# Performance work log

Hardware: AMD Instinct MI355X
Metric: run time of the kernel (lower is better)

## Reference

```python
import jax, jax.numpy as jnp
import numpy as np

B, S, HID = 2, 2048, 2048
H = 16           # num_attention_heads
DH = 192         # head_dim
DR = 64          # qk_rope_head_dim
DN = DH - DR     # qk_nope_head_dim
Q_LORA = 512
ROPE_THETA = 10000.0
EPS = 1e-6


def setup_inputs() -> dict:
    key = jax.random.key(0)
    ks = jax.random.split(key, 8)
    scale = 0.02
    x = jax.random.normal(ks[0], (B, S, HID), dtype=jnp.float32)
    position_ids = jnp.broadcast_to(jnp.arange(S, dtype=jnp.int64), (B, S))
    w_qa = jax.random.normal(ks[1], (HID, Q_LORA), dtype=jnp.float32) * scale
    q_norm_w = jnp.ones((Q_LORA,), dtype=jnp.float32)
    w_qb = jax.random.normal(ks[2], (Q_LORA, H * DH), dtype=jnp.float32) * scale
    w_k = jax.random.normal(ks[3], (HID, DH), dtype=jnp.float32) * scale
    w_v = jax.random.normal(ks[4], (HID, DH), dtype=jnp.float32) * scale
    w_o = jax.random.normal(ks[5], (H * DH, HID), dtype=jnp.float32) * scale
    attn_sink = jax.random.normal(ks[6], (H,), dtype=jnp.float32)
    return {"x": x, "w_qa": w_qa, "q_norm_w": q_norm_w, "w_qb": w_qb,
            "w_k": w_k, "w_v": w_v, "w_o": w_o, "attn_sink": attn_sink,
            "position_ids": position_ids}


def _rms_norm(h, w):
    var = jnp.mean(jnp.square(h), axis=-1, keepdims=True)
    return h * jax.lax.rsqrt(var + EPS) * w


def _rotate_half(t):
    t1, t2 = jnp.split(t, 2, axis=-1)
    return jnp.concatenate([-t2, t1], axis=-1)


def _rope_cos_sin(position_ids, dtype):
    inv_freq = 1.0 / (ROPE_THETA ** (jnp.arange(0, DR, 2, dtype=jnp.float32) / DR))
    freqs = position_ids.astype(jnp.float32)[:, :, None] * inv_freq[None, None, :]  # [B,S,DR/2]
    emb = jnp.concatenate([freqs, freqs], axis=-1)  # [B,S,DR]
    return jnp.cos(emb).astype(dtype), jnp.sin(emb).astype(dtype)


def reference(x, w_qa, q_norm_w, w_qb, w_k, w_v, w_o, attn_sink, position_ids):
    b, s, _ = x.shape
    # Low-rank Q path: q_a -> RMSNorm -> q_b, reshape to heads
    q_a = _rms_norm(x @ w_qa, q_norm_w)                      # [B,S,Q_LORA]
    q = (q_a @ w_qb).reshape(b, s, H, DH).transpose(0, 2, 1, 3)  # [B,H,S,DH]
    # MQA single KV head
    k = (x @ w_k)[:, None]                                    # [B,1,S,DH]
    v = (x @ w_v)[:, None]                                    # [B,1,S,DH]
    # Decoupled RoPE on trailing DR dims of q and k
    cos, sin = _rope_cos_sin(position_ids, x.dtype)           # [B,S,DR]
    cos4, sin4 = cos[:, None], sin[:, None]                   # [B,1,S,DR]
    q_nope, q_rope = q[..., :DN], q[..., DN:]
    k_nope, k_rope = k[..., :DN], k[..., DN:]
    q_rope = q_rope * cos4 + _rotate_half(q_rope) * sin4
    k_rope = k_rope * cos4 + _rotate_half(k_rope) * sin4
    q = jnp.concatenate([q_nope, q_rope], axis=-1)
    k = jnp.concatenate([k_nope, k_rope], axis=-1)
    # Attention with learned sink logit
    scaling = DH ** -0.5
    scores = jnp.einsum("bhsd,bgtd->bhst", q, k) * scaling    # [B,H,S,S]
    neg_inf = jnp.finfo(scores.dtype).min
    causal = jnp.tril(jnp.ones((s, s), dtype=bool))
    scores = jnp.where(causal[None, None], scores, neg_inf)
    sink = jnp.broadcast_to(attn_sink.reshape(1, H, 1, 1), (b, H, s, 1)).astype(scores.dtype)
    scores = jnp.concatenate([scores, sink], axis=-1)         # [B,H,S,S+1]
    probs = jax.nn.softmax(scores, axis=-1)[..., :-1]          # drop sink column
    attn = jnp.einsum("bhst,bgtd->bhsd", probs, v)            # [B,H,S,DH]
    attn = attn.transpose(0, 2, 1, 3).reshape(b, s, H * DH)
    return attn @ w_o
```

## Files before the change

### kernel.cpp

```cpp
#include <hip/hip_runtime.h>
#include <hip/hip_bf16.h>

typedef __bf16 bf16_t;
typedef __bf16 bf16x8 __attribute__((ext_vector_type(8)));
typedef __bf16 bf16x4 __attribute__((ext_vector_type(4)));
typedef float  f32x4  __attribute__((ext_vector_type(4)));
typedef __attribute__((address_space(3))) unsigned int lds_u32_t;
typedef __attribute__((address_space(1))) const unsigned int glb_u32_t;

#define B_    2
#define S_    2048
#define HID_  2048
#define H_    16
#define DH_   192
#define DR_   64
#define DN_   128
#define QL_   512
#define NROWS (B_*S_)
#define QKD   (H_*DH_)

#if __has_builtin(__builtin_amdgcn_exp2f)
#define EXP2(x) __builtin_amdgcn_exp2f(x)
#else
#define EXP2(x) exp2f(x)
#endif

__device__ inline void xcd_remap(int& bx, int& by) {
  const int gx = gridDim.x;
  const int nwg = gx * gridDim.y;
  const int flat = by * gx + bx;
  const int q = nwg >> 3;
  const int nf = (flat & 7) * q + (flat >> 3);
  bx = nf % gx;
  by = nf / gx;
}

__global__ void cast_f32_to_bf16(const float* __restrict__ in, bf16_t* __restrict__ out, int n4) {
  int i = blockIdx.x * blockDim.x + threadIdx.x;
  if (i >= n4) return;
  const float4 v = reinterpret_cast<const float4*>(in)[i];
  bf16x4 r;
  r[0] = (bf16_t)v.x; r[1] = (bf16_t)v.y; r[2] = (bf16_t)v.z; r[3] = (bf16_t)v.w;
  reinterpret_cast<bf16x4*>(out)[i] = r;
}

__global__ __launch_bounds__(256) void transpose_all(
    const float* __restrict__ i0, const float* __restrict__ i1,
    const float* __restrict__ i2, const float* __restrict__ i3,
    const float* __restrict__ i4,
    bf16_t* __restrict__ o0, bf16_t* __restrict__ o1, bf16_t* __restrict__ o2,
    bf16_t* __restrict__ o3, bf16_t* __restrict__ o4) {
  int id = blockIdx.x;
  const float* in; bf16_t* out; int R, C, lid;
  if (id < 1024)      { in = i0; out = o0; R = 2048; C = 512;  lid = id; }
  else if (id < 2560) { in = i1; out = o1; R = 512;  C = 3072; lid = id - 1024; }
  else if (id < 2944) { in = i2; out = o2; R = 2048; C = 192;  lid = id - 2560; }
  else if (id < 3328) { in = i3; out = o3; R = 2048; C = 192;  lid = id - 2944; }
  else                { in = i4; out = o4; R = 3072; C = 2048; lid = id - 3328; }
  const int cw = C >> 5;
  const int c0 = (lid % cw) * 32, r0 = (lid / cw) * 32;
  __shared__ float t[32][33];
  const int tx = threadIdx.x & 31;
  const int ty = threadIdx.x >> 5;
#pragma unroll
  for (int j = 0; j < 4; ++j)
    t[ty + j * 8][tx] = in[(size_t)(r0 + ty + j * 8) * C + c0 + tx];
  __syncthreads();
#pragma unroll
  for (int j = 0; j < 4; ++j)
    out[(size_t)(c0 + ty + j * 8) * R + r0 + tx] = (bf16_t)t[tx][ty + j * 8];
}

#define BM 64
#define BN 64
#define BK 64
#define LDT 72

__global__ __launch_bounds__(256) void gemm_kv_kernel(
    const bf16_t* __restrict__ A, const bf16_t* __restrict__ BT,
    bf16_t* __restrict__ Kout, bf16_t* __restrict__ VTout) {
  __shared__ __align__(16) bf16_t sA[BM][LDT];
  __shared__ __align__(16) bf16_t sB[BN][LDT];
  const int tid = threadIdx.x;
  const int w  = tid >> 6;
  const int l  = tid & 63;
  const int lg = l >> 4, lr = l & 15;
  int bx = blockIdx.x, by = blockIdx.y;
  xcd_remap(bx, by);
  const int m0 = by * BM, n0 = bx * BN;
  const int K = HID_;

  f32x4 acc[4];
#pragma unroll
  for (int c = 0; c < 4; ++c) acc[c] = f32x4{0.f, 0.f, 0.f, 0.f};

  for (int k0 = 0; k0 < K; k0 += BK) {
#pragma unroll
    for (int i = 0; i < 2; ++i) {
      int cid = tid + i * 256;
      int row = cid >> 3;
      int cb  = (cid & 7) * 8;
      *reinterpret_cast<uint4*>(&sA[row][cb]) =
          *reinterpret_cast<const uint4*>(&A[(size_t)(m0 + row) * K + k0 + cb]);
      *reinterpret_cast<uint4*>(&sB[row][cb]) =
          *reinterpret_cast<const uint4*>(&BT[(size_t)(n0 + row) * K + k0 + cb]);
    }
    __syncthreads();
#pragma unroll
    for (int ks = 0; ks < 2; ++ks) {
      bf16x8 af = *reinterpret_cast<const bf16x8*>(&sA[w * 16 + lr][ks * 32 + lg * 8]);
#pragma unroll
      for (int c = 0; c < 4; ++c) {
        bf16x8 bfr = *reinterpret_cast<const bf16x8*>(&sB[c * 16 + lr][ks * 32 + lg * 8]);
        acc[c] = __builtin_amdgcn_mfma_f32_16x16x32_bf16(af, bfr, acc[c], 0, 0, 0);
      }
    }
    __syncthreads();
  }
#pragma unroll
  for (int c = 0; c < 4; ++c) {
#pragma unroll
    for (int r = 0; r < 4; ++r) {
      int row = m0 + w * 16 + lg * 4 + r;
      int col = n0 + c * 16 + lr;
      float v = acc[c][r];
      if (col < DH_) Kout[(size_t)row * DH_ + col] = (bf16_t)v;
      else           VTout[(size_t)(col - DH_) * NROWS + row] = (bf16_t)v;
    }
  }
}

template<int OMODE>
__global__ __launch_bounds__(256) void gemm128_kernel(
    const bf16_t* __restrict__ A, const bf16_t* __restrict__ BT,
    void* __restrict__ C, int M, int N, int K, float oscale) {
  __shared__ __align__(16) bf16_t sA[128 * 64];
  __shared__ __align__(16) bf16_t sB[128 * 64];
  const int tid = threadIdx.x;
  const int w  = tid >> 6;
  const int l  = tid & 63;
  const int lg = l >> 4, lr = l & 15;
  const int wm = w >> 1, wn = w & 1;
  int bx = blockIdx.x, by = blockIdx.y;
  xcd_remap(bx, by);
  const int m0 = by * 128, n0 = bx * 128;

  size_t aoff[4], boff[4];
  int ldsoff[4];
#pragma unroll
  for (int i = 0; i < 4; ++i) {
    int cid = i * 256 + tid;
    int row = cid >> 3, ch = cid & 7;
    int sch = ch ^ (row & 7);
    aoff[i] = (size_t)(m0 + row) * K + sch * 8;
    boff[i] = (size_t)(n0 + row) * K + sch * 8;
    ldsoff[i] = (i * 256 + w * 64) * 8;
  }

  f32x4 acc[4][4];
#pragma unroll
  for (int mi = 0; mi < 4; ++mi)
#pragma unroll
    for (int ni = 0; ni < 4; ++ni) acc[mi][ni] = f32x4{0.f, 0.f, 0.f, 0.f};

  for (int k0 = 0; k0 < K; k0 += 64) {
#pragma unroll
    for (int i = 0; i < 4; ++i) {
      __builtin_amdgcn_global_load_lds((glb_u32_t*)(A + aoff[i] + k0),
                                       (lds_u32_t*)(sA + ldsoff[i]), 16, 0, 0);
      __builtin_amdgcn_global_load_lds((glb_u32_t*)(BT + boff[i] + k0),
                                       (lds_u32_t*)(sB + ldsoff[i]), 16, 0, 0);
    }
    asm volatile("s_waitcnt vmcnt(0)" ::: "memory");
    __syncthreads();

#pragma unroll
    for (int ks = 0; ks < 2; ++ks) {
      bf16x8 af[4], bfr[4];
#pragma unroll
      for (int mi = 0; mi < 4; ++mi) {
        int row = wm * 64 + mi * 16 + lr;
        af[mi] = *reinterpret_cast<const bf16x8*>(
            sA + row * 64 + (((ks * 4 + lg) ^ (row & 7)) << 3));
      }
#pragma unroll
      for (int ni = 0; ni < 4; ++ni) {
        int row = wn * 64 + ni * 16 + lr;
        bfr[ni] = *reinterpret_cast<const bf16x8*>(
            sB + row * 64 + (((ks * 4 + lg) ^ (row & 7)) << 3));
      }
#pragma unroll
      for (int mi = 0; mi < 4; ++mi)
#pragma unroll
        for (int ni = 0; ni < 4; ++ni)
          acc[mi][ni] = __builtin_amdgcn_mfma_f32_16x16x32_bf16(af[mi], bfr[ni], acc[mi][ni], 0, 0, 0);
    }
    __syncthreads();
  }

#pragma unroll
  for (int mi = 0; mi < 4; ++mi) {
#pragma unroll
    for (int ni = 0; ni < 4; ++ni) {
#pragma unroll
      for (int r = 0; r < 4; ++r) {
        int row = m0 + wm * 64 + mi * 16 + lg * 4 + r;
        int col = n0 + wn * 64 + ni * 16 + lr;
        float v = acc[mi][ni][r];
        if (OMODE == 0) ((float*)C)[(size_t)row * N + col]  = v;
        else            ((bf16_t*)C)[(size_t)row * N + col] = (bf16_t)(v * oscale);
      }
    }
  }
}

template<int OMODE>
__global__ __launch_bounds__(256) void gemm64x128_kernel(
    const bf16_t* __restrict__ A, const bf16_t* __restrict__ BT,
    void* __restrict__ C, int M, int N, int K, float oscale) {
  __shared__ __align__(16) bf16_t sA[64 * 64];
  __shared__ __align__(16) bf16_t sB[128 * 64];
  const int tid = threadIdx.x;
  const int w  = tid >> 6;
  const int l  = tid & 63;
  const int lg = l >> 4, lr = l & 15;
  const int wm = w >> 1, wn = w & 1;
  int bx = blockIdx.x, by = blockIdx.y;
  xcd_remap(bx, by);
  const int m0 = by * 64, n0 = bx * 128;

  size_t aoff[2], boff[4];
  int ldsa[2], ldsb[4];
#pragma unroll
  for (int i = 0; i < 2; ++i) {
    int cid = i * 256 + tid;
    int row = cid >> 3, ch = cid & 7;
    aoff[i] = (size_t)(m0 + row) * K + (ch ^ (row & 7)) * 8;
    ldsa[i] = (i * 256 + w * 64) * 8;
  }
#pragma unroll
  for (int i = 0; i < 4; ++i) {
    int cid = i * 256 + tid;
    int row = cid >> 3, ch = cid & 7;
    boff[i] = (size_t)(n0 + row) * K + (ch ^ (row & 7)) * 8;
    ldsb[i] = (i * 256 + w * 64) * 8;
  }

  f32x4 acc[2][4];
#pragma unroll
  for (int mi = 0; mi < 2; ++mi)
#pragma unroll
    for (int ni = 0; ni < 4; ++ni) acc[mi][ni] = f32x4{0.f, 0.f, 0.f, 0.f};

  for (int k0 = 0; k0 < K; k0 += 64) {
#pragma unroll
    for (int i = 0; i < 2; ++i)
      __builtin_amdgcn_global_load_lds((glb_u32_t*)(A + aoff[i] + k0),
                                       (lds_u32_t*)(sA + ldsa[i]), 16, 0, 0);
#pragma unroll
    for (int i = 0; i < 4; ++i)
      __builtin_amdgcn_global_load_lds((glb_u32_t*)(BT + boff[i] + k0),
                                       (lds_u32_t*)(sB + ldsb[i]), 16, 0, 0);
    asm volatile("s_waitcnt vmcnt(0)" ::: "memory");
    __syncthreads();

#pragma unroll
    for (int ks = 0; ks < 2; ++ks) {
      bf16x8 af[2], bfr[4];
#pragma unroll
      for (int mi = 0; mi < 2; ++mi) {
        int row = wm * 32 + mi * 16 + lr;
        af[mi] = *reinterpret_cast<const bf16x8*>(
            sA + row * 64 + (((ks * 4 + lg) ^ (row & 7)) << 3));
      }
#pragma unroll
      for (int ni = 0; ni < 4; ++ni) {
        int row = wn * 64 + ni * 16 + lr;
        bfr[ni] = *reinterpret_cast<const bf16x8*>(
            sB + row * 64 + (((ks * 4 + lg) ^ (row & 7)) << 3));
      }
#pragma unroll
      for (int mi = 0; mi < 2; ++mi)
#pragma unroll
        for (int ni = 0; ni < 4; ++ni)
          acc[mi][ni] = __builtin_amdgcn_mfma_f32_16x16x32_bf16(af[mi], bfr[ni], acc[mi][ni], 0, 0, 0);
    }
    __syncthreads();
  }

#pragma unroll
  for (int mi = 0; mi < 2; ++mi) {
#pragma unroll
    for (int ni = 0; ni < 4; ++ni) {
#pragma unroll
      for (int r = 0; r < 4; ++r) {
        int row = m0 + wm * 32 + mi * 16 + lg * 4 + r;
        int col = n0 + wn * 64 + ni * 16 + lr;
        float v = acc[mi][ni][r];
        if (OMODE == 0) ((float*)C)[(size_t)row * N + col]  = v;
        else            ((bf16_t*)C)[(size_t)row * N + col] = (bf16_t)(v * oscale);
      }
    }
  }
}

__global__ __launch_bounds__(64) void rmsnorm_kernel(bf16_t* __restrict__ qa,
                                                     const float* __restrict__ wnorm) {
  int row = blockIdx.x;
  int l = threadIdx.x;
  bf16x8 v = *reinterpret_cast<const bf16x8*>(&qa[(size_t)row * QL_ + l * 8]);
  float f[8];
  float ss = 0.f;
#pragma unroll
  for (int e = 0; e < 8; ++e) { f[e] = (float)v[e]; ss += f[e] * f[e]; }
#pragma unroll
  for (int off = 32; off >= 1; off >>= 1) ss += __shfl_xor(ss, off);
  float rstd = rsqrtf(ss * (1.0f / 512.0f) + 1e-6f);
  bf16x8 o;
#pragma unroll
  for (int e = 0; e < 8; ++e) o[e] = (bf16_t)(f[e] * rstd * wnorm[l * 8 + e]);
  *reinterpret_cast<bf16x8*>(&qa[(size_t)row * QL_ + l * 8]) = o;
}

__global__ void rope_kernel(bf16_t* __restrict__ q, bf16_t* __restrict__ k) {
  int idx = blockIdx.x * blockDim.x + threadIdx.x;
  const int NQ = NROWS * H_ * 32;
  if (idx < NQ) {
    int d   = idx & 31;
    int h   = (idx >> 5) & 15;
    int row = idx >> 9;
    int s = row & (S_ - 1);
    float freq = (float)s * expf(-(float)d * (9.210340371976184f / 32.0f));
    float sn, cs;
    sincosf(freq, &sn, &cs);
    size_t base = (size_t)row * QKD + h * DH_ + DN_ + d;
    float q1 = (float)q[base], q2 = (float)q[base + 32];
    q[base]      = (bf16_t)(q1 * cs - q2 * sn);
    q[base + 32] = (bf16_t)(q2 * cs + q1 * sn);
  } else {
    int i2 = idx - NQ;
    if (i2 >= NROWS * 32) return;
    int d   = i2 & 31;
    int row = i2 >> 5;
    int s = row & (S_ - 1);
    float freq = (float)s * expf(-(float)d * (9.210340371976184f / 32.0f));
    float sn, cs;
    sincosf(freq, &sn, &cs);
    size_t base = (size_t)row * DH_ + DN_ + d;
    float k1 = (float)k[base], k2 = (float)k[base + 32];
    k[base]      = (bf16_t)(k1 * cs - k2 * sn);
    k[base + 32] = (bf16_t)(k2 * cs + k1 * sn);
  }
}

#define KB32  32
#define SPLD  40

__global__ __launch_bounds__(256, 2) void attn_kernel(
    const bf16_t* __restrict__ q, const bf16_t* __restrict__ k,
    const bf16_t* __restrict__ vt, const float* __restrict__ sink,
    bf16_t* __restrict__ attn) {
  __shared__ __align__(16) bf16_t sK[2][KB32 * DH_];
  __shared__ __align__(16) bf16_t sV[DH_ * KB32];
  __shared__ __align__(16) bf16_t sP[4][32][SPLD];
  const int tid = threadIdx.x;
  const int w  = tid >> 6;
  const int l  = tid & 63;
  const int lg = l >> 4, lr = l & 15;
  const int qx = blockIdx.x >> 5;
  const int qt = (qx < 8) ? (15 - qx) : (qx - 8);
  const int bh = blockIdx.x & 31;
  const int b  = bh >> 4, h = bh & 15;
  const int wrow0 = qt * 128 + w * 32;
  const int ktmax_w = 4 * qt + w;
  const int ktmax_b = 4 * qt + 3;

  const bf16_t* kb  = k  + (size_t)(b * S_) * DH_;
  const bf16_t* vtb = vt + (size_t)(b * S_);

  int koff[3], voff[3], ldst[3];
#pragma unroll
  for (int i = 0; i < 3; ++i) {
    int g = i * 256 + tid;
    int krow = g / 24, kch = g - krow * 24;
    koff[i] = krow * DH_ + ((kch ^ (krow & 7)) << 3);
    int vrow = g >> 2, vch = g & 3;
    voff[i] = vrow * NROWS + ((vch ^ (vrow & 3)) << 3);
    ldst[i] = (i * 256 + w * 64) * 8;
  }

  auto stageK = [&](int kt, int bu) {
    const bf16_t* ksrc = kb + (size_t)kt * KB32 * DH_;
#pragma unroll
    for (int i = 0; i < 3; ++i)
      __builtin_amdgcn_global_load_lds((glb_u32_t*)(ksrc + koff[i]),
                                       (lds_u32_t*)(&sK[bu][0] + ldst[i]), 16, 0, 0);
  };
  auto stageV = [&](int kt) {
    const bf16_t* vsrc = vtb + kt * KB32;
#pragma unroll
    for (int i = 0; i < 3; ++i)
      __builtin_amdgcn_global_load_lds((glb_u32_t*)(vsrc + voff[i]),
                                       (lds_u32_t*)(sV + ldst[i]), 16, 0, 0);
  };

  bf16x8 qf[2][6];
#pragma unroll
  for (int rf = 0; rf < 2; ++rf) {
    size_t rowoff = (size_t)(b * S_ + wrow0 + rf * 16 + lr) * QKD + h * DH_;
#pragma unroll
    for (int ks = 0; ks < 6; ++ks)
      qf[rf][ks] = *reinterpret_cast<const bf16x8*>(&q[rowoff + ks * 32 + lg * 8]);
  }

  bf16x8 vones;
#pragma unroll
  for (int e = 0; e < 8; ++e) vones[e] = (bf16_t)((lr == 0) ? 1.0f : 0.0f);

  f32x4 acc[2][13];
#pragma unroll
  for (int rf = 0; rf < 2; ++rf) {
#pragma unroll
    for (int c = 0; c < 12; ++c) acc[rf][c] = f32x4{0.f, 0.f, 0.f, 0.f};
    float init = (lr == 0) ? 1.0f : 0.0f;
    acc[rf][12] = f32x4{init, init, init, init};
  }

  const float L2E = 1.4426950408889634f;
  float m[2][4];
  float sk2 = sink[h] * L2E;
#pragma unroll
  for (int rf = 0; rf < 2; ++rf)
#pragma unroll
    for (int r = 0; r < 4; ++r) m[rf][r] = sk2;

  stageK(0, 0);
  int cur = 0;

  for (int kt = 0; kt <= ktmax_b; ++kt) {
    __syncthreads();

    stageV(kt);
    const bool more = (kt < ktmax_b);
    if (more) stageK(kt + 1, cur ^ 1);

    if (kt <= ktmax_w) {
      if (more) { asm volatile("s_waitcnt vmcnt(6)" ::: "memory"); }
      else      { asm volatile("s_waitcnt vmcnt(3)" ::: "memory"); }

      f32x4 sc[2][2];
#pragma unroll
      for (int rf = 0; rf < 2; ++rf)
#pragma unroll
        for (int c = 0; c < 2; ++c) sc[rf][c] = f32x4{0.f, 0.f, 0.f, 0.f};
#pragma unroll
      for (int c = 0; c < 2; ++c) {
        const int row = c * 16 + lr;
        const int rx  = row & 7;
        const bf16_t* kr = &sK[cur][0] + row * DH_;
#pragma unroll
        for (int ks = 0; ks < 6; ++ks) {
          bf16x8 kf = *reinterpret_cast<const bf16x8*>(kr + (((ks * 4 + lg) ^ rx) << 3));
          sc[0][c] = __builtin_amdgcn_mfma_f32_16x16x32_bf16(qf[0][ks], kf, sc[0][c], 0, 0, 0);
          sc[1][c] = __builtin_amdgcn_mfma_f32_16x16x32_bf16(qf[1][ks], kf, sc[1][c], 0, 0, 0);
        }
      }

      if (kt == ktmax_w) {
#pragma unroll
        for (int rf = 0; rf < 2; ++rf)
#pragma unroll
          for (int c = 0; c < 2; ++c)
#pragma unroll
            for (int r = 0; r < 4; ++r)
              if ((kt * 32 + c * 16 + lr) > (wrow0 + rf * 16 + lg * 4 + r))
                sc[rf][c][r] = -1e30f;
      }

      int ok = 1;
      float lmax[2][4];
#pragma unroll
      for (int rf = 0; rf < 2; ++rf)
#pragma unroll
        for (int r = 0; r < 4; ++r) {
          lmax[rf][r] = fmaxf(sc[rf][0][r], sc[rf][1][r]);
          ok &= (lmax[rf][r] <= m[rf][r] + 8.0f);
        }
      if (!__all(ok)) {
#pragma unroll
        for (int rf = 0; rf < 2; ++rf) {
          float rmax[4], alpha[4];
#pragma unroll
          for (int r = 0; r < 4; ++r) rmax[r] = lmax[rf][r];
#pragma unroll
          for (int off = 1; off < 16; off <<= 1) {
#pragma unroll
            for (int r = 0; r < 4; ++r) rmax[r] = fmaxf(rmax[r], __shfl_xor(rmax[r], off));
          }
#pragma unroll
          for (int r = 0; r < 4; ++r) {
            float mn = fmaxf(m[rf][r], rmax[r]);
            alpha[r] = EXP2(m[rf][r] - mn);
            m[rf][r] = mn;
          }
#pragma unroll
          for (int c = 0; c < 13; ++c)
#pragma unroll
            for (int r = 0; r < 4; ++r) acc[rf][c][r] *= alpha[r];
        }
      }

#pragma unroll
      for (int rf = 0; rf < 2; ++rf)
#pragma unroll
        for (int c = 0; c < 2; ++c)
#pragma unroll
          for (int r = 0; r < 4; ++r)
            sP[w][rf * 16 + lg * 4 + r][c * 16 + lr] = (bf16_t)EXP2(sc[rf][c][r] - m[rf][r]);

      if (more) { asm volatile("s_waitcnt vmcnt(3)" ::: "memory"); }
      else      { asm volatile("s_waitcnt vmcnt(0)" ::: "memory"); }

      bf16x8 pf[2];
      pf[0] = *reinterpret_cast<const bf16x8*>(&sP[w][lr][lg * 8]);
      pf[1] = *reinterpret_cast<const bf16x8*>(&sP[w][16 + lr][lg * 8]);
#pragma unroll
      for (int c2 = 0; c2 < 12; ++c2) {
        const int row = c2 * 16 + lr;
        bf16x8 vf = *reinterpret_cast<const bf16x8*>(
            sV + row * KB32 + ((lg ^ (row & 3)) << 3));
        acc[0][c2] = __builtin_amdgcn_mfma_f32_16x16x32_bf16(pf[0], vf, acc[0][c2], 0, 0, 0);
        acc[1][c2] = __builtin_amdgcn_mfma_f32_16x16x32_bf16(pf[1], vf, acc[1][c2], 0, 0, 0);
      }
      acc[0][12] = __builtin_amdgcn_mfma_f32_16x16x32_bf16(pf[0], vones, acc[0][12], 0, 0, 0);
      acc[1][12] = __builtin_amdgcn_mfma_f32_16x16x32_bf16(pf[1], vones, acc[1][12], 0, 0, 0);
    }
    cur ^= 1;
  }

#pragma unroll
  for (int rf = 0; rf < 2; ++rf) {
    float rl[4];
#pragma unroll
    for (int r = 0; r < 4; ++r) rl[r] = 1.0f / __shfl(acc[rf][12][r], l & 48);
#pragma unroll
    for (int c2 = 0; c2 < 12; ++c2) {
#pragma unroll
      for (int r = 0; r < 4; ++r) {
        int i = wrow0 + rf * 16 + lg * 4 + r;
        size_t off = (size_t)(b * S_ + i) * QKD + h * DH_ + c2 * 16 + lr;
        attn[off] = (bf16_t)(acc[rf][c2][r] * rl[r]);
      }
    }
  }
}

extern "C" void kernel_launch(void* const* d_in, const int* in_sizes, int n_in,
                              void* d_out, int out_size, void* d_ws, size_t ws_size,
                              hipStream_t stream) {
  const float* x        = (const float*)d_in[0];
  const float* w_qa     = (const float*)d_in[1];
  const float* q_norm_w = (const float*)d_in[2];
  const float* w_qb     = (const float*)d_in[3];
  const float* w_k      = (const float*)d_in[4];
  const float* w_v      = (const float*)d_in[5];
  const float* w_o      = (const float*)d_in[6];
  const float* attn_sink= (const float*)d_in[7];
  float* out = (float*)d_out;

  char* ws = (char*)d_ws;
  size_t off = 0;
  auto alloc = [&](size_t bytes) -> void* {
    void* p = ws + off;
    off += (bytes + 255) & ~(size_t)255;
    return p;
  };
  bf16_t* q_b  = (bf16_t*)alloc((size_t)NROWS * QKD * 2);
  bf16_t* k_b  = (bf16_t*)alloc((size_t)NROWS * DH_ * 2);
  bf16_t* vt_b = (bf16_t*)alloc((size_t)DH_ * NROWS * 2);
  bf16_t* wo_t = (bf16_t*)alloc((size_t)HID_ * QKD * 2);
  size_t temp_start = off;
  bf16_t* xb    = (bf16_t*)alloc((size_t)NROWS * HID_ * 2);
  bf16_t* wqa_t = (bf16_t*)alloc((size_t)QL_ * HID_ * 2);
  bf16_t* wqb_t = (bf16_t*)alloc((size_t)QKD * QL_ * 2);
  bf16_t* wkv_t = (bf16_t*)alloc((size_t)(2 * DH_) * HID_ * 2);
  bf16_t* qa_b  = (bf16_t*)alloc((size_t)NROWS * QL_ * 2);
  bf16_t* attn_b = (bf16_t*)(ws + temp_start);

  const float SCALE2 = 0.10411754646447386f;

  int n4x = (int)((size_t)NROWS * HID_ / 4);
  cast_f32_to_bf16<<<dim3((n4x + 255) / 256), dim3(256), 0, stream>>>(x, xb, n4x);
  transpose_all<<<dim3(9472), dim3(256), 0, stream>>>(
      w_qa, w_qb, w_k, w_v, w_o,
      wqa_t, wqb_t, wkv_t, wkv_t + (size_t)DH_ * HID_, wo_t);

  gemm64x128_kernel<1><<<dim3(QL_ / 128, NROWS / 64), 256, 0, stream>>>(xb, wqa_t, qa_b, NROWS, QL_, HID_, 1.0f);
  rmsnorm_kernel<<<dim3(NROWS), dim3(64), 0, stream>>>(qa_b, q_norm_w);
  gemm128_kernel<1><<<dim3(QKD / 128, NROWS / 128), 256, 0, stream>>>(qa_b, wqb_t, q_b, NROWS, QKD, QL_, SCALE2);
  gemm_kv_kernel<<<dim3((2 * DH_) / BN, NROWS / BM), 256, 0, stream>>>(xb, wkv_t, k_b, vt_b);
  {
    int total = NROWS * (H_ + 1) * 32;
    rope_kernel<<<dim3((total + 255) / 256), dim3(256), 0, stream>>>(q_b, k_b);
  }
  attn_kernel<<<dim3(512), dim3(256), 0, stream>>>(q_b, k_b, vt_b, attn_sink, attn_b);
  gemm64x128_kernel<0><<<dim3(HID_ / 128, NROWS / 64), 256, 0, stream>>>(attn_b, wo_t, out, NROWS, HID_, QKD, 1.0f);
}
```

Baseline: 293.7 us.

## Split long causal attention tiles across two blocks and fuse RoPE into GEMM epilogues

The eight longest query tiles now have their key range split across two blocks. Each half writes unnormalized partial outputs plus max and denominator, and a new merge kernel combines them. This balances the triangular causal workload across 768 blocks instead of 512. Separately, RoPE moves into the epilogues of the Q and K GEMMs, removing the standalone rope kernel and its extra read/write pass. The cost is extra partial-output traffic in bf16 and one additional kernel launch.

```diff
diff --git a/kernel.cpp b/kernel.cpp
--- a/kernel.cpp
+++ b/kernel.cpp
@@ -117,6 +117,23 @@
     }
     __syncthreads();
   }
+
+  if (n0 == 128) {
+#pragma unroll
+    for (int c = 0; c < 2; ++c) {
+      const float invf = expf((float)(c * 16 + lr) * (-9.210340371976184f / 32.0f));
+#pragma unroll
+      for (int r = 0; r < 4; ++r) {
+        int s = (m0 + w * 16 + lg * 4 + r) & (S_ - 1);
+        float sn, cs;
+        sincosf((float)s * invf, &sn, &cs);
+        float x1 = acc[c][r], x2 = acc[c + 2][r];
+        acc[c][r]     = x1 * cs - x2 * sn;
+        acc[c + 2][r] = x2 * cs + x1 * sn;
+      }
+    }
+  }
+
 #pragma unroll
   for (int c = 0; c < 4; ++c) {
 #pragma unroll
@@ -130,7 +147,7 @@
   }
 }
 
-template<int OMODE>
+template<int OMODE, bool ROPE>
 __global__ __launch_bounds__(256) void gemm128_kernel(
     const bf16_t* __restrict__ A, const bf16_t* __restrict__ BT,
     void* __restrict__ C, int M, int N, int K, float oscale) {
@@ -196,6 +213,31 @@
           acc[mi][ni] = __builtin_amdgcn_mfma_f32_16x16x32_bf16(af[mi], bfr[ni], acc[mi][ni], 0, 0, 0);
     }
     __syncthreads();
+  }
+
+  if (ROPE) {
+    const int t = 2 * bx + wn;
+    if (t >= 2 && (t - 2) % 3 == 0) {
+      float invf[2];
+#pragma unroll
+      for (int ni = 0; ni < 2; ++ni)
+        invf[ni] = expf((float)(ni * 16 + lr) * (-9.210340371976184f / 32.0f));
+#pragma unroll
+      for (int mi = 0; mi < 4; ++mi) {
+#pragma unroll
+        for (int ni = 0; ni < 2; ++ni) {
+#pragma unroll
+          for (int r = 0; r < 4; ++r) {
+            int s = (m0 + wm * 64 + mi * 16 + lg * 4 + r) & (S_ - 1);
+            float sn, cs;
+            sincosf((float)s * invf[ni], &sn, &cs);
+            float x1 = acc[mi][ni][r], x2 = acc[mi][ni + 2][r];
+            acc[mi][ni][r]     = x1 * cs - x2 * sn;
+            acc[mi][ni + 2][r] = x2 * cs + x1 * sn;
+          }
+        }
+      }
+    }
   }
 
 #pragma unroll
@@ -322,44 +364,14 @@
   *reinterpret_cast<bf16x8*>(&qa[(size_t)row * QL_ + l * 8]) = o;
 }
 
-__global__ void rope_kernel(bf16_t* __restrict__ q, bf16_t* __restrict__ k) {
-  int idx = blockIdx.x * blockDim.x + threadIdx.x;
-  const int NQ = NROWS * H_ * 32;
-  if (idx < NQ) {
-    int d   = idx & 31;
-    int h   = (idx >> 5) & 15;
-    int row = idx >> 9;
-    int s = row & (S_ - 1);
-    float freq = (float)s * expf(-(float)d * (9.210340371976184f / 32.0f));
-    float sn, cs;
-    sincosf(freq, &sn, &cs);
-    size_t base = (size_t)row * QKD + h * DH_ + DN_ + d;
-    float q1 = (float)q[base], q2 = (float)q[base + 32];
-    q[base]      = (bf16_t)(q1 * cs - q2 * sn);
-    q[base + 32] = (bf16_t)(q2 * cs + q1 * sn);
-  } else {
-    int i2 = idx - NQ;
-    if (i2 >= NROWS * 32) return;
-    int d   = i2 & 31;
-    int row = i2 >> 5;
-    int s = row & (S_ - 1);
-    float freq = (float)s * expf(-(float)d * (9.210340371976184f / 32.0f));
-    float sn, cs;
-    sincosf(freq, &sn, &cs);
-    size_t base = (size_t)row * DH_ + DN_ + d;
-    float k1 = (float)k[base], k2 = (float)k[base + 32];
-    k[base]      = (bf16_t)(k1 * cs - k2 * sn);
-    k[base + 32] = (bf16_t)(k2 * cs + k1 * sn);
-  }
-}
-
 #define KB32  32
 #define SPLD  40
 
 __global__ __launch_bounds__(256, 2) void attn_kernel(
     const bf16_t* __restrict__ q, const bf16_t* __restrict__ k,
     const bf16_t* __restrict__ vt, const float* __restrict__ sink,
-    bf16_t* __restrict__ attn) {
+    bf16_t* __restrict__ attn, bf16_t* __restrict__ Opart,
+    float* __restrict__ mpart, float* __restrict__ dpart) {
   __shared__ __align__(16) bf16_t sK[2][KB32 * DH_];
   __shared__ __align__(16) bf16_t sV[DH_ * KB32];
   __shared__ __align__(16) bf16_t sP[4][32][SPLD];
@@ -367,13 +379,31 @@
   const int w  = tid >> 6;
   const int l  = tid & 63;
   const int lg = l >> 4, lr = l & 15;
-  const int qx = blockIdx.x >> 5;
-  const int qt = (qx < 8) ? (15 - qx) : (qx - 8);
-  const int bh = blockIdx.x & 31;
-  const int b  = bh >> 4, h = bh & 15;
+
+  const int id = blockIdx.x;
+  int qt, bh, lo, hib;
+  bool split, sink0;
+  if (id < 512) {
+    split = true;
+    qt = 15 - (id >> 6);
+    int r2 = id & 63;
+    bh = r2 >> 1;
+    int chunk = r2 & 1;
+    int Kiters = 4 * qt + 4, Hh = Kiters >> 1;
+    lo  = chunk ? Hh : 0;
+    hib = chunk ? (Kiters - 1) : (Hh - 1);
+    sink0 = (chunk == 0);
+  } else {
+    split = false;
+    int j = id - 512;
+    qt = 7 - (j >> 5);
+    bh = j & 31;
+    lo = 0; hib = 4 * qt + 3;
+    sink0 = true;
+  }
+  const int b = bh >> 4, h = bh & 15;
   const int wrow0 = qt * 128 + w * 32;
   const int ktmax_w = 4 * qt + w;
-  const int ktmax_b = 4 * qt + 3;
 
   const bf16_t* kb  = k  + (size_t)(b * S_) * DH_;
   const bf16_t* vtb = vt + (size_t)(b * S_);
@@ -422,26 +452,26 @@
   for (int rf = 0; rf < 2; ++rf) {
 #pragma unroll
     for (int c = 0; c < 12; ++c) acc[rf][c] = f32x4{0.f, 0.f, 0.f, 0.f};
-    float init = (lr == 0) ? 1.0f : 0.0f;
+    float init = (sink0 && lr == 0) ? 1.0f : 0.0f;
     acc[rf][12] = f32x4{init, init, init, init};
   }
 
   const float L2E = 1.4426950408889634f;
   float m[2][4];
-  float sk2 = sink[h] * L2E;
+  float m0v = sink0 ? (sink[h] * L2E) : -1e30f;
 #pragma unroll
   for (int rf = 0; rf < 2; ++rf)
 #pragma unroll
-    for (int r = 0; r < 4; ++r) m[rf][r] = sk2;
-
-  stageK(0, 0);
+    for (int r = 0; r < 4; ++r) m[rf][r] = m0v;
+
+  stageK(lo, 0);
   int cur = 0;
 
-  for (int kt = 0; kt <= ktmax_b; ++kt) {
+  for (int kt = lo; kt <= hib; ++kt) {
     __syncthreads();
 
     stageV(kt);
-    const bool more = (kt < ktmax_b);
+    const bool more = (kt < hib);
     if (more) stageK(kt + 1, cur ^ 1);
 
     if (kt <= ktmax_w) {
@@ -538,20 +568,71 @@
     cur ^= 1;
   }
 
-#pragma unroll
-  for (int rf = 0; rf < 2; ++rf) {
-    float rl[4];
-#pragma unroll
-    for (int r = 0; r < 4; ++r) rl[r] = 1.0f / __shfl(acc[rf][12][r], l & 48);
-#pragma unroll
-    for (int c2 = 0; c2 < 12; ++c2) {
-#pragma unroll
-      for (int r = 0; r < 4; ++r) {
-        int i = wrow0 + rf * 16 + lg * 4 + r;
-        size_t off = (size_t)(b * S_ + i) * QKD + h * DH_ + c2 * 16 + lr;
-        attn[off] = (bf16_t)(acc[rf][c2][r] * rl[r]);
-      }
-    }
+  if (!split) {
+#pragma unroll
+    for (int rf = 0; rf < 2; ++rf) {
+      float rl[4];
+#pragma unroll
+      for (int r = 0; r < 4; ++r) rl[r] = 1.0f / __shfl(acc[rf][12][r], l & 48);
+#pragma unroll
+      for (int c2 = 0; c2 < 12; ++c2) {
+#pragma unroll
+        for (int r = 0; r < 4; ++r) {
+          int i = wrow0 + rf * 16 + lg * 4 + r;
+          size_t off = (size_t)(b * S_ + i) * QKD + h * DH_ + c2 * 16 + lr;
+          attn[off] = (bf16_t)(acc[rf][c2][r] * rl[r]);
+        }
+      }
+    }
+  } else {
+    const int slot = id;
+#pragma unroll
+    for (int rf = 0; rf < 2; ++rf) {
+#pragma unroll
+      for (int c2 = 0; c2 < 12; ++c2) {
+#pragma unroll
+        for (int r = 0; r < 4; ++r) {
+          int rowl = w * 32 + rf * 16 + lg * 4 + r;
+          Opart[(size_t)slot * (128 * 192) + rowl * 192 + c2 * 16 + lr] = (bf16_t)acc[rf][c2][r];
+        }
+      }
+      if (lr == 0) {
+#pragma unroll
+        for (int r = 0; r < 4; ++r) {
+          int rowl = w * 32 + rf * 16 + lg * 4 + r;
+          mpart[slot * 128 + rowl] = m[rf][r];
+          dpart[slot * 128 + rowl] = acc[rf][12][r];
+        }
+      }
+    }
+  }
+}
+
+__global__ __launch_bounds__(256) void attn_merge(
+    const bf16_t* __restrict__ Opart, const float* __restrict__ mpart,
+    const float* __restrict__ dpart, bf16_t* __restrict__ attn) {
+  const int t  = blockIdx.x;
+  const int qt = 8 + (t >> 5), bh = t & 31;
+  const int b = bh >> 4, h = bh & 15;
+  const int base = (15 - qt) * 64 + bh * 2;
+  const size_t offA = (size_t)base * (128 * 192);
+  const size_t offB = offA + 128 * 192;
+  const int rbA = base * 128, rbB = rbA + 128;
+  for (int c = threadIdx.x; c < 3072; c += 256) {
+    int row = c / 24, col8 = (c - row * 24) * 8;
+    float mA = mpart[rbA + row], mB = mpart[rbB + row];
+    float dA = dpart[rbA + row], dB = dpart[rbB + row];
+    float M = fmaxf(mA, mB);
+    float wA = EXP2(mA - M), wB = EXP2(mB - M);
+    float rden = 1.0f / (wA * dA + wB * dB);
+    bf16x8 va = *reinterpret_cast<const bf16x8*>(&Opart[offA + row * 192 + col8]);
+    bf16x8 vb = *reinterpret_cast<const bf16x8*>(&Opart[offB + row * 192 + col8]);
+    bf16x8 o;
+#pragma unroll
+    for (int e = 0; e < 8; ++e)
+      o[e] = (bf16_t)((wA * (float)va[e] + wB * (float)vb[e]) * rden);
+    size_t off = (size_t)(b * S_ + qt * 128 + row) * QKD + h * DH_ + col8;
+    *reinterpret_cast<bf16x8*>(&attn[off]) = o;
   }
 }
 
@@ -586,6 +667,9 @@
   bf16_t* wkv_t = (bf16_t*)alloc((size_t)(2 * DH_) * HID_ * 2);
   bf16_t* qa_b  = (bf16_t*)alloc((size_t)NROWS * QL_ * 2);
   bf16_t* attn_b = (bf16_t*)(ws + temp_start);
+  bf16_t* opart = (bf16_t*)alloc((size_t)512 * 128 * 192 * 2);
+  float*  mpart = (float*)alloc((size_t)512 * 128 * 4);
+  float*  dpart = (float*)alloc((size_t)512 * 128 * 4);
 
   const float SCALE2 = 0.10411754646447386f;
 
@@ -597,12 +681,10 @@
 
   gemm64x128_kernel<1><<<dim3(QL_ / 128, NROWS / 64), 256, 0, stream>>>(xb, wqa_t, qa_b, NROWS, QL_, HID_, 1.0f);
   rmsnorm_kernel<<<dim3(NROWS), dim3(64), 0, stream>>>(qa_b, q_norm_w);
-  gemm128_kernel<1><<<dim3(QKD / 128, NROWS / 128), 256, 0, stream>>>(qa_b, wqb_t, q_b, NROWS, QKD, QL_, SCALE2);
+  gemm128_kernel<1, true><<<dim3(QKD / 128, NROWS / 128), 256, 0, stream>>>(qa_b, wqb_t, q_b, NROWS, QKD, QL_, SCALE2);
   gemm_kv_kernel<<<dim3((2 * DH_) / BN, NROWS / BM), 256, 0, stream>>>(xb, wkv_t, k_b, vt_b);
-  {
-    int total = NROWS * (H_ + 1) * 32;
-    rope_kernel<<<dim3((total + 255) / 256), dim3(256), 0, stream>>>(q_b, k_b);
-  }
-  attn_kernel<<<dim3(512), dim3(256), 0, stream>>>(q_b, k_b, vt_b, attn_sink, attn_b);
+  attn_kernel<<<dim3(768), dim3(256), 0, stream>>>(q_b, k_b, vt_b, attn_sink,
+                                                   attn_b, opart, mpart, dpart);
+  attn_merge<<<dim3(256), dim3(256), 0, stream>>>(opart, mpart, dpart, attn_b);
   gemm64x128_kernel<0><<<dim3(HID_ / 128, NROWS / 64), 256, 0, stream>>>(attn_b, wo_t, out, NROWS, HID_, QKD, 1.0f);
 }
```

After: 315.2 us. 7.3% more time.

## Fuse RoPE into Q and KV GEMM epilogues and merge prep kernels

Applied to the files above, without the earlier changes.

Applies rotary embedding directly to the fp32 accumulators in the epilogues of the Q-projection GEMM and the KV GEMM, so the standalone rope kernel and its bf16 read-modify-write of Q and K go away. The x cast is also folded into the weight transpose kernel as extra blocks, removing one launch. The epilogue selects the rope column tiles by tile index, which depends on 64-column warp tiles lining up with the 192-wide head layout. RoPE is now applied before the bf16 rounding, which changes numerics slightly.

```diff
diff --git a/kernel.cpp b/kernel.cpp
--- a/kernel.cpp
+++ b/kernel.cpp
@@ -35,22 +35,28 @@
   by = nf / gx;
 }
 
-__global__ void cast_f32_to_bf16(const float* __restrict__ in, bf16_t* __restrict__ out, int n4) {
-  int i = blockIdx.x * blockDim.x + threadIdx.x;
-  if (i >= n4) return;
-  const float4 v = reinterpret_cast<const float4*>(in)[i];
-  bf16x4 r;
-  r[0] = (bf16_t)v.x; r[1] = (bf16_t)v.y; r[2] = (bf16_t)v.z; r[3] = (bf16_t)v.w;
-  reinterpret_cast<bf16x4*>(out)[i] = r;
-}
-
-__global__ __launch_bounds__(256) void transpose_all(
+__global__ __launch_bounds__(256) void prep_all(
     const float* __restrict__ i0, const float* __restrict__ i1,
     const float* __restrict__ i2, const float* __restrict__ i3,
-    const float* __restrict__ i4,
+    const float* __restrict__ i4, const float* __restrict__ xin,
     bf16_t* __restrict__ o0, bf16_t* __restrict__ o1, bf16_t* __restrict__ o2,
-    bf16_t* __restrict__ o3, bf16_t* __restrict__ o4) {
+    bf16_t* __restrict__ o3, bf16_t* __restrict__ o4, bf16_t* __restrict__ xout) {
   int id = blockIdx.x;
+  if (id >= 9472) {
+    const int lid = id - 9472;
+    const float4* src = reinterpret_cast<const float4*>(xin);
+    bf16x4* dst = reinterpret_cast<bf16x4*>(xout);
+    const int base = lid * 1024;
+#pragma unroll
+    for (int j = 0; j < 4; ++j) {
+      int idx = base + j * 256 + threadIdx.x;
+      float4 v = src[idx];
+      bf16x4 r;
+      r[0] = (bf16_t)v.x; r[1] = (bf16_t)v.y; r[2] = (bf16_t)v.z; r[3] = (bf16_t)v.w;
+      dst[idx] = r;
+    }
+    return;
+  }
   const float* in; bf16_t* out; int R, C, lid;
   if (id < 1024)      { in = i0; out = o0; R = 2048; C = 512;  lid = id; }
   else if (id < 2560) { in = i1; out = o1; R = 512;  C = 3072; lid = id - 1024; }
@@ -117,6 +123,23 @@
     }
     __syncthreads();
   }
+
+  if (n0 == 128) {
+#pragma unroll
+    for (int c = 0; c < 2; ++c) {
+      const float invf = expf((float)(c * 16 + lr) * (-9.210340371976184f / 32.0f));
+#pragma unroll
+      for (int r = 0; r < 4; ++r) {
+        int s = (m0 + w * 16 + lg * 4 + r) & (S_ - 1);
+        float sn, cs;
+        sincosf((float)s * invf, &sn, &cs);
+        float x1 = acc[c][r], x2 = acc[c + 2][r];
+        acc[c][r]     = x1 * cs - x2 * sn;
+        acc[c + 2][r] = x2 * cs + x1 * sn;
+      }
+    }
+  }
+
 #pragma unroll
   for (int c = 0; c < 4; ++c) {
 #pragma unroll
@@ -130,7 +153,7 @@
   }
 }
 
-template<int OMODE>
+template<int OMODE, bool ROPE>
 __global__ __launch_bounds__(256) void gemm128_kernel(
     const bf16_t* __restrict__ A, const bf16_t* __restrict__ BT,
     void* __restrict__ C, int M, int N, int K, float oscale) {
@@ -196,6 +219,31 @@
           acc[mi][ni] = __builtin_amdgcn_mfma_f32_16x16x32_bf16(af[mi], bfr[ni], acc[mi][ni], 0, 0, 0);
     }
     __syncthreads();
+  }
+
+  if (ROPE) {
+    const int t = 2 * bx + wn;
+    if (t >= 2 && (t - 2) % 3 == 0) {
+      float invf[2];
+#pragma unroll
+      for (int ni = 0; ni < 2; ++ni)
+        invf[ni] = expf((float)(ni * 16 + lr) * (-9.210340371976184f / 32.0f));
+#pragma unroll
+      for (int mi = 0; mi < 4; ++mi) {
+#pragma unroll
+        for (int ni = 0; ni < 2; ++ni) {
+#pragma unroll
+          for (int r = 0; r < 4; ++r) {
+            int s = (m0 + wm * 64 + mi * 16 + lg * 4 + r) & (S_ - 1);
+            float sn, cs;
+            sincosf((float)s * invf[ni], &sn, &cs);
+            float x1 = acc[mi][ni][r], x2 = acc[mi][ni + 2][r];
+            acc[mi][ni][r]     = x1 * cs - x2 * sn;
+            acc[mi][ni + 2][r] = x2 * cs + x1 * sn;
+          }
+        }
+      }
+    }
   }
 
 #pragma unroll
@@ -320,37 +368,6 @@
 #pragma unroll
   for (int e = 0; e < 8; ++e) o[e] = (bf16_t)(f[e] * rstd * wnorm[l * 8 + e]);
   *reinterpret_cast<bf16x8*>(&qa[(size_t)row * QL_ + l * 8]) = o;
-}
-
-__global__ void rope_kernel(bf16_t* __restrict__ q, bf16_t* __restrict__ k) {
-  int idx = blockIdx.x * blockDim.x + threadIdx.x;
-  const int NQ = NROWS * H_ * 32;
-  if (idx < NQ) {
-    int d   = idx & 31;
-    int h   = (idx >> 5) & 15;
-    int row = idx >> 9;
-    int s = row & (S_ - 1);
-    float freq = (float)s * expf(-(float)d * (9.210340371976184f / 32.0f));
-    float sn, cs;
-    sincosf(freq, &sn, &cs);
-    size_t base = (size_t)row * QKD + h * DH_ + DN_ + d;
-    float q1 = (float)q[base], q2 = (float)q[base + 32];
-    q[base]      = (bf16_t)(q1 * cs - q2 * sn);
-    q[base + 32] = (bf16_t)(q2 * cs + q1 * sn);
-  } else {
-    int i2 = idx - NQ;
-    if (i2 >= NROWS * 32) return;
-    int d   = i2 & 31;
-    int row = i2 >> 5;
-    int s = row & (S_ - 1);
-    float freq = (float)s * expf(-(float)d * (9.210340371976184f / 32.0f));
-    float sn, cs;
-    sincosf(freq, &sn, &cs);
-    size_t base = (size_t)row * DH_ + DN_ + d;
-    float k1 = (float)k[base], k2 = (float)k[base + 32];
-    k[base]      = (bf16_t)(k1 * cs - k2 * sn);
-    k[base + 32] = (bf16_t)(k2 * cs + k1 * sn);
-  }
 }
 
 #define KB32  32
@@ -589,20 +606,14 @@
 
   const float SCALE2 = 0.10411754646447386f;
 
-  int n4x = (int)((size_t)NROWS * HID_ / 4);
-  cast_f32_to_bf16<<<dim3((n4x + 255) / 256), dim3(256), 0, stream>>>(x, xb, n4x);
-  transpose_all<<<dim3(9472), dim3(256), 0, stream>>>(
-      w_qa, w_qb, w_k, w_v, w_o,
-      wqa_t, wqb_t, wkv_t, wkv_t + (size_t)DH_ * HID_, wo_t);
+  prep_all<<<dim3(11520), dim3(256), 0, stream>>>(
+      w_qa, w_qb, w_k, w_v, w_o, x,
+      wqa_t, wqb_t, wkv_t, wkv_t + (size_t)DH_ * HID_, wo_t, xb);
 
   gemm64x128_kernel<1><<<dim3(QL_ / 128, NROWS / 64), 256, 0, stream>>>(xb, wqa_t, qa_b, NROWS, QL_, HID_, 1.0f);
   rmsnorm_kernel<<<dim3(NROWS), dim3(64), 0, stream>>>(qa_b, q_norm_w);
-  gemm128_kernel<1><<<dim3(QKD / 128, NROWS / 128), 256, 0, stream>>>(qa_b, wqb_t, q_b, NROWS, QKD, QL_, SCALE2);
+  gemm128_kernel<1, true><<<dim3(QKD / 128, NROWS / 128), 256, 0, stream>>>(qa_b, wqb_t, q_b, NROWS, QKD, QL_, SCALE2);
   gemm_kv_kernel<<<dim3((2 * DH_) / BN, NROWS / BM), 256, 0, stream>>>(xb, wkv_t, k_b, vt_b);
-  {
-    int total = NROWS * (H_ + 1) * 32;
-    rope_kernel<<<dim3((total + 255) / 256), dim3(256), 0, stream>>>(q_b, k_b);
-  }
   attn_kernel<<<dim3(512), dim3(256), 0, stream>>>(q_b, k_b, vt_b, attn_sink, attn_b);
   gemm64x128_kernel<0><<<dim3(HID_ / 128, NROWS / 64), 256, 0, stream>>>(attn_b, wo_t, out, NROWS, HID_, QKD, 1.0f);
 }
```

Result: slower. 304.5 us (+3.7%).
